# Kernel optimization log

Measured on AMD Instinct MI355X. Metric: run time of the kernel, lower is better.

Reference implementation:

```python
import jax, jax.numpy as jnp
import numpy as np

EYE_PENALTY = 1.0e6


def setup_inputs() -> dict:
    key = jax.random.key(0)
    k1, k2 = jax.random.split(key)
    B, NIN, NK, DK = 512, 1024, 128, 5
    x = jax.random.normal(k1, (B, NIN), dtype=jnp.float32)
    theta = jax.random.normal(k2, (NIN, NK, DK), dtype=jnp.float32) * 0.05
    log_weight_scale = jnp.zeros((NK, DK), dtype=jnp.float32)
    bias = jnp.full((NK,), -1.0, dtype=jnp.float32)
    return {"x": x, "theta": theta, "log_weight_scale": log_weight_scale, "bias": bias}


def reference(x, theta, log_weight_scale, bias):
    # kernel = theta * exp(log_weight_scale) / ||theta||_2 (norm over input dim)
    l2 = jnp.sqrt(jnp.sum(theta * theta, axis=0))            # [K, D]
    kernel = theta * (jnp.exp(log_weight_scale) / l2)[None]   # [NIN, K, D]
    actv = jnp.einsum('bi,ikd->bkd', x, kernel)               # [B, K, D]
    B = x.shape[0]
    # all-pairs L1 distance per kernel: [B, K, B]
    diff = actv[:, :, :, None] - jnp.transpose(actv, (1, 2, 0))[None]  # [B,K,D,B]
    abs_dif = jnp.sum(jnp.abs(diff), axis=2)                  # [B, K, B]
    abs_dif = abs_dif + EYE_PENALTY * jnp.eye(B, dtype=x.dtype)[:, None, :]
    f = jnp.sum(jnp.exp(-abs_dif), axis=2) + bias[None, :]    # [B, K]
    return jnp.concatenate([x, f], axis=1)                    # [B, NIN + K]
```

## Files before the change

kernel.cpp:

```cpp
#include <hip/hip_runtime.h>
#include <hip/hip_fp16.h>
#include <math.h>

constexpr int B    = 512;
constexpr int NIN  = 1024;
constexpr int NK   = 128;
constexpr int DK   = 5;
constexpr int NF   = NK * DK;
constexpr int NOUT = NIN + NK;
constexpr int SPLITK = 8;
constexpr int LDA = 136;
#define LOG2E 1.44269504088896f

typedef _Float16 f16x4 __attribute__((ext_vector_type(4)));
typedef _Float16 f16x8 __attribute__((ext_vector_type(8)));
typedef float    f32x4 __attribute__((ext_vector_type(4)));

__global__ __launch_bounds__(256) void gemm_kernel(
        const float* __restrict__ x,
        const float* __restrict__ theta,
        __half* __restrict__ actvP16,
        float* __restrict__ ps) {
    __shared__ _Float16 Ath[32 * LDA];
    __shared__ _Float16 Bxh[64 * LDA];
    __shared__ float    red2[32][33];

    const int t    = threadIdx.x;
    const int tile = blockIdx.x >> 3;
    const int z    = blockIdx.x & 7;
    const int nt   = tile >> 3;
    const int bt   = tile & 7;
    const int n0   = nt * 32;
    const int b0   = bt * 64;
    const bool do_ps = (bt == 0);
    const int kw   = z * 128;

    const int kq = t >> 3;
    const int nc = (t & 7) * 4;
    float4 tv0 = *(const float4*)&theta[(kw + kq*4 + 0) * NF + n0 + nc];
    float4 tv1 = *(const float4*)&theta[(kw + kq*4 + 1) * NF + n0 + nc];
    float4 tv2 = *(const float4*)&theta[(kw + kq*4 + 2) * NF + n0 + nc];
    float4 tv3 = *(const float4*)&theta[(kw + kq*4 + 3) * NF + n0 + nc];

    const int br = t >> 2;
    const int ki = t & 3;
    float4 xv[8];
    #pragma unroll
    for (int i = 0; i < 8; ++i)
        xv[i] = *(const float4*)&x[(b0 + br) * NIN + kw + (ki + i * 4) * 4];

    if (do_ps) {
        red2[kq][nc + 0] = tv0.x*tv0.x + tv1.x*tv1.x + tv2.x*tv2.x + tv3.x*tv3.x;
        red2[kq][nc + 1] = tv0.y*tv0.y + tv1.y*tv1.y + tv2.y*tv2.y + tv3.y*tv3.y;
        red2[kq][nc + 2] = tv0.z*tv0.z + tv1.z*tv1.z + tv2.z*tv2.z + tv3.z*tv3.z;
        red2[kq][nc + 3] = tv0.w*tv0.w + tv1.w*tv1.w + tv2.w*tv2.w + tv3.w*tv3.w;
    }

    {
        f16x4 h;
        h[0]=(_Float16)tv0.x; h[1]=(_Float16)tv1.x; h[2]=(_Float16)tv2.x; h[3]=(_Float16)tv3.x;
        *(f16x4*)&Ath[(nc + 0) * LDA + kq * 4] = h;
        h[0]=(_Float16)tv0.y; h[1]=(_Float16)tv1.y; h[2]=(_Float16)tv2.y; h[3]=(_Float16)tv3.y;
        *(f16x4*)&Ath[(nc + 1) * LDA + kq * 4] = h;
        h[0]=(_Float16)tv0.z; h[1]=(_Float16)tv1.z; h[2]=(_Float16)tv2.z; h[3]=(_Float16)tv3.z;
        *(f16x4*)&Ath[(nc + 2) * LDA + kq * 4] = h;
        h[0]=(_Float16)tv0.w; h[1]=(_Float16)tv1.w; h[2]=(_Float16)tv2.w; h[3]=(_Float16)tv3.w;
        *(f16x4*)&Ath[(nc + 3) * LDA + kq * 4] = h;
    }
    #pragma unroll
    for (int i = 0; i < 8; ++i) {
        f16x4 h;
        h[0] = (_Float16)xv[i].x;  h[1] = (_Float16)xv[i].y;
        h[2] = (_Float16)xv[i].z;  h[3] = (_Float16)xv[i].w;
        *(f16x4*)&Bxh[br * LDA + (ki + i * 4) * 4] = h;
    }
    __syncthreads();

    const int w   = t >> 6;
    const int l   = t & 63;
    const int r16 = l & 15;
    const int kg  = l >> 4;

    f32x4 acc0 = {0.f,0.f,0.f,0.f}, acc1 = {0.f,0.f,0.f,0.f};
    #pragma unroll
    for (int ks = 0; ks < 4; ++ks) {
        const f16x8 bv  = *(const f16x8*)&Bxh[(w*16 + r16)*LDA + ks*32 + kg*8];
        const f16x8 av0 = *(const f16x8*)&Ath[( 0 + r16)*LDA + ks*32 + kg*8];
        const f16x8 av1 = *(const f16x8*)&Ath[(16 + r16)*LDA + ks*32 + kg*8];
        acc0 = __builtin_amdgcn_mfma_f32_16x16x32_f16(av0, bv, acc0, 0, 0, 0);
        acc1 = __builtin_amdgcn_mfma_f32_16x16x32_f16(av1, bv, acc1, 0, 0, 0);
    }

    {
        __half* dst = actvP16 + (size_t)z * NF * B
                    + (size_t)(n0 + kg*4) * B + b0 + w*16 + r16;
        #pragma unroll
        for (int j = 0; j < 4; ++j) {
            dst[j*B]          = __float2half(acc0[j]);
            dst[(16 + j) * B] = __float2half(acc1[j]);
        }
    }
    if (do_ps) {
        __syncthreads();
        if (t < 32) {
            float tot = 0.f;
            #pragma unroll
            for (int rr = 0; rr < 32; ++rr) tot += red2[rr][t];
            ps[z * NF + n0 + t] = tot;
        }
    }
}

__global__ __launch_bounds__(1024, 8) void pairwise_kernel(
        const __half* __restrict__ actvP16,
        const float* __restrict__ ps,
        const float* __restrict__ lws,
        const float* __restrict__ bias,
        const float* __restrict__ x,
        float* __restrict__ out) {
    __shared__ __half a16s[DK * B];
    __shared__ float  red[8 * 128];
    __shared__ float  s_sh[DK];
    __shared__ float  red_ps[DK * SPLITK];

    const int k = blockIdx.x;
    const int e = blockIdx.y;
    const int t = threadIdx.x;

    if (t >= 512 && t < 768) {
        const int u = t - 512;
        const int row = k * 4 + e;
        ((float4*)out)[row * (NOUT/4) + u] = ((const float4*)x)[row * (NIN/4) + u];
    }
    if (t >= 768 && t < 768 + DK * SPLITK) {
        const int u = t - 768;
        red_ps[u] = ps[(u / DK) * NF + k * DK + (u % DK)];
    }

    const size_t slab = (size_t)k * DK * B;
    float accf[8];
    #pragma unroll
    for (int i = 0; i < 8; ++i) accf[i] = 0.f;
    if (t < 320) {
        #pragma unroll
        for (int z = 0; z < SPLITK; ++z) {
            const f16x8 v = *(const f16x8*)(actvP16 + (size_t)z * NF * B + slab + t * 8);
            #pragma unroll
            for (int i = 0; i < 8; ++i) accf[i] += (float)v[i];
        }
    }
    __syncthreads();
    if (t < DK) {
        float sum = 0.f;
        #pragma unroll
        for (int c = 0; c < SPLITK; ++c) sum += red_ps[c * DK + t];
        s_sh[t] = __expf(lws[k * DK + t]) * rsqrtf(sum) * LOG2E;
    }
    __syncthreads();
    if (t < 320) {
        const float s = s_sh[t >> 6];
        f16x8 h;
        #pragma unroll
        for (int i = 0; i < 8; ++i) h[i] = (_Float16)(accf[i] * s);
        *(f16x8*)&a16s[t * 8] = h;
    }
    __syncthreads();

    const int g  = t >> 7;
    const int r  = t & 127;
    const int ba = e * 128 + r;

    __half2 A2[DK];
    #pragma unroll
    for (int d = 0; d < DK; ++d) A2[d] = __half2half2(a16s[d * B + ba]);

    float acc = 0.f;
    const int bp0 = g * 64;

    union W8 { f16x8 v; __half2 h[4]; };
    typedef _Float16 f16x2v __attribute__((ext_vector_type(2)));
    union HV { __half2 h; f16x2v v; };
    const HV ones = {__half2half2(__float2half(1.0f))};

    #pragma unroll 2
    for (int m = 0; m < 8; ++m) {
        const int bp = bp0 + m * 8;
        W8 w0, w1, w2, w3, w4;
        w0.v = *(const f16x8*)&a16s[0*B + bp];
        w1.v = *(const f16x8*)&a16s[1*B + bp];
        w2.v = *(const f16x8*)&a16s[2*B + bp];
        w3.v = *(const f16x8*)&a16s[3*B + bp];
        w4.v = *(const f16x8*)&a16s[4*B + bp];
        #pragma unroll
        for (int c = 0; c < 4; ++c) {
            __half2 dA = __habs2(__hsub2(A2[0], w0.h[c]));
            dA = __hadd2(dA, __habs2(__hsub2(A2[1], w1.h[c])));
            dA = __hadd2(dA, __habs2(__hsub2(A2[2], w2.h[c])));
            dA = __hadd2(dA, __habs2(__hsub2(A2[3], w3.h[c])));
            dA = __hadd2(dA, __habs2(__hsub2(A2[4], w4.h[c])));
            HV eA; eA.h = h2exp2(__hneg2(dA));
#if __has_builtin(__builtin_amdgcn_fdot2)
            acc = __builtin_amdgcn_fdot2(eA.v, ones.v, acc, false);
#else
            acc += __low2float(eA.h) + __high2float(eA.h);
#endif
        }
    }
    red[g * 128 + r] = acc;
    __syncthreads();
    if (t < 128) {
        float f = -1.0f + bias[k];
        #pragma unroll
        for (int gg = 0; gg < 8; ++gg) f += red[gg * 128 + t];
        out[(e * 128 + t) * NOUT + NIN + k] = f;
    }
}

extern "C" void kernel_launch(void* const* d_in, const int* in_sizes, int n_in,
                              void* d_out, int out_size, void* d_ws, size_t ws_size,
                              hipStream_t stream) {
    const float* x     = (const float*)d_in[0];
    const float* theta = (const float*)d_in[1];
    const float* lws   = (const float*)d_in[2];
    const float* bias  = (const float*)d_in[3];
    float* out = (float*)d_out;

    char* wsb = (char*)d_ws;
    float*  ps       = (float*)wsb;
    __half* actvP16  = (__half*)(wsb + (64 << 10));

    gemm_kernel<<<dim3(1280), 256, 0, stream>>>(x, theta, actvP16, ps);
    pairwise_kernel<<<dim3(NK, 4), 1024, 0, stream>>>(actvP16, ps, lws, bias, x, out);
}
```

Before: 24.90 us.

## Register-block pairwise kernel over 4 anchor rows per thread with fp32 exp2

Each thread in the pairwise kernel now handles 4 anchor rows against 32 partners, so every shared-memory partner vector it reads is reused four times. The grid is halved to 2 row-blocks of 256 per kernel, and the copy of x into the output is spread across more threads. The half2 exp2 plus fdot2 accumulation is replaced by fp32 hardware exp2 on each half, which doubles the transcendental count per pair but may give better precision. Fewer blocks and more registers per thread could lower parallelism and occupancy.

```diff
diff --git a/kernel.cpp b/kernel.cpp
--- a/kernel.cpp
+++ b/kernel.cpp
@@ -111,7 +111,7 @@
     }
 }
 
-__global__ __launch_bounds__(1024, 8) void pairwise_kernel(
+__global__ __launch_bounds__(1024, 4) void pairwise_kernel(
         const __half* __restrict__ actvP16,
         const float* __restrict__ ps,
         const float* __restrict__ lws,
@@ -119,7 +119,7 @@
         const float* __restrict__ x,
         float* __restrict__ out) {
     __shared__ __half a16s[DK * B];
-    __shared__ float  red[8 * 128];
+    __shared__ float  red[16 * 256];
     __shared__ float  s_sh[DK];
     __shared__ float  red_ps[DK * SPLITK];
 
@@ -127,13 +127,14 @@
     const int e = blockIdx.y;
     const int t = threadIdx.x;
 
-    if (t >= 512 && t < 768) {
+    if (t >= 512) {
         const int u = t - 512;
-        const int row = k * 4 + e;
-        ((float4*)out)[row * (NOUT/4) + u] = ((const float4*)x)[row * (NIN/4) + u];
-    }
-    if (t >= 768 && t < 768 + DK * SPLITK) {
-        const int u = t - 768;
+        const int row = k * 4 + e * 2 + (u >> 8);
+        const int c4  = u & 255;
+        ((float4*)out)[row * (NOUT/4) + c4] = ((const float4*)x)[row * (NIN/4) + c4];
+    }
+    if (t >= 320 && t < 320 + DK * SPLITK) {
+        const int u = t - 320;
         red_ps[u] = ps[(u / DK) * NF + k * DK + (u % DK)];
     }
 
@@ -166,24 +167,23 @@
     }
     __syncthreads();
 
-    const int g  = t >> 7;
-    const int r  = t & 127;
-    const int ba = e * 128 + r;
-
-    __half2 A2[DK];
-    #pragma unroll
-    for (int d = 0; d < DK; ++d) A2[d] = __half2half2(a16s[d * B + ba]);
-
-    float acc = 0.f;
-    const int bp0 = g * 64;
+    const int w  = t >> 6;
+    const int l  = t & 63;
+    const int ba = e * 256 + l * 4;
+
+    __half2 A2[4][DK];
+    #pragma unroll
+    for (int j = 0; j < 4; ++j)
+        #pragma unroll
+        for (int d = 0; d < DK; ++d)
+            A2[j][d] = __half2half2(a16s[d * B + ba + j]);
+
+    float acc[4] = {0.f, 0.f, 0.f, 0.f};
+    const int bp0 = w * 32;
 
     union W8 { f16x8 v; __half2 h[4]; };
-    typedef _Float16 f16x2v __attribute__((ext_vector_type(2)));
-    union HV { __half2 h; f16x2v v; };
-    const HV ones = {__half2half2(__float2half(1.0f))};
-
-    #pragma unroll 2
-    for (int m = 0; m < 8; ++m) {
+    #pragma unroll
+    for (int m = 0; m < 4; ++m) {
         const int bp = bp0 + m * 8;
         W8 w0, w1, w2, w3, w4;
         w0.v = *(const f16x8*)&a16s[0*B + bp];
@@ -193,26 +193,30 @@
         w4.v = *(const f16x8*)&a16s[4*B + bp];
         #pragma unroll
         for (int c = 0; c < 4; ++c) {
-            __half2 dA = __habs2(__hsub2(A2[0], w0.h[c]));
-            dA = __hadd2(dA, __habs2(__hsub2(A2[1], w1.h[c])));
-            dA = __hadd2(dA, __habs2(__hsub2(A2[2], w2.h[c])));
-            dA = __hadd2(dA, __habs2(__hsub2(A2[3], w3.h[c])));
-            dA = __hadd2(dA, __habs2(__hsub2(A2[4], w4.h[c])));
-            HV eA; eA.h = h2exp2(__hneg2(dA));
-#if __has_builtin(__builtin_amdgcn_fdot2)
-            acc = __builtin_amdgcn_fdot2(eA.v, ones.v, acc, false);
-#else
-            acc += __low2float(eA.h) + __high2float(eA.h);
-#endif
-        }
-    }
-    red[g * 128 + r] = acc;
-    __syncthreads();
-    if (t < 128) {
+            #pragma unroll
+            for (int j = 0; j < 4; ++j) {
+                __half2 dA = __habs2(__hsub2(A2[j][0], w0.h[c]));
+                dA = __hadd2(dA, __habs2(__hsub2(A2[j][1], w1.h[c])));
+                dA = __hadd2(dA, __habs2(__hsub2(A2[j][2], w2.h[c])));
+                dA = __hadd2(dA, __habs2(__hsub2(A2[j][3], w3.h[c])));
+                dA = __hadd2(dA, __habs2(__hsub2(A2[j][4], w4.h[c])));
+                const float lo = __low2float(dA);
+                const float hi = __high2float(dA);
+                acc[j] += __builtin_amdgcn_exp2f(-lo);
+                acc[j] += __builtin_amdgcn_exp2f(-hi);
+            }
+        }
+    }
+    #pragma unroll
+    for (int j = 0; j < 4; ++j)
+        red[w * 256 + (l * 4 + j)] = acc[j];
+    __syncthreads();
+
+    if (t < 256) {
         float f = -1.0f + bias[k];
         #pragma unroll
-        for (int gg = 0; gg < 8; ++gg) f += red[gg * 128 + t];
-        out[(e * 128 + t) * NOUT + NIN + k] = f;
+        for (int gg = 0; gg < 16; ++gg) f += red[gg * 256 + t];
+        out[(size_t)(e * 256 + t) * NOUT + NIN + k] = f;
     }
 }
 
@@ -230,5 +234,5 @@
     __half* actvP16  = (__half*)(wsb + (64 << 10));
 
     gemm_kernel<<<dim3(1280), 256, 0, stream>>>(x, theta, actvP16, ps);
-    pairwise_kernel<<<dim3(NK, 4), 1024, 0, stream>>>(actvP16, ps, lws, bias, x, out);
+    pairwise_kernel<<<dim3(NK, 2), 1024, 0, stream>>>(actvP16, ps, lws, bias, x, out);
 }
```

New measurement: 24.63 us. Within noise of the previous version (-1.1%).
